# Performance work log

Hardware: AMD Instinct MI355X
Metric: run time of the kernel (lower is better)

Reference implementation:

```python
import jax, jax.numpy as jnp
import numpy as np

N_CLUSTERS = 10

def _conv(x, w, b, stride):
    y = jax.lax.conv_general_dilated(x, w, stride, 'VALID', dimension_numbers=('NCHW', 'OIHW', 'NCHW'))
    return y + b[None, :, None, None]

def _forward(x, conv1_w, conv1_b, conv2_w, conv2_b, conv3_w, conv3_b,
             anc0_w, anc0_b, anc1_w, anc1_b, anc2_w, anc2_b, anc3_w, anc3_b,
             W1_w, W1_b, U_w, U_b, V_w, V_b, Wa_w, Wa_b,
             cluster_w, cluster_b, cls_w, cls_b):
    # backbone: three stride-2 valid convs
    h1 = _conv(x, conv1_w, conv1_b, (2, 2))
    h2 = _conv(h1, conv2_w, conv2_b, (2, 2))
    h3 = _conv(h2, conv3_w, conv3_b, (2, 2))  # [1,512,63,63]
    ancs = [_conv(h3, anc0_w, anc0_b, (1, 1)),
            _conv(h3, anc1_w, anc1_b, (1, 1)),
            _conv(h3, anc2_w, anc2_b, (1, 1)),
            _conv(h3, anc3_w, anc3_b, (1, 1))]
    ksizes = [(3, 3), (1, 1), (3, 1), (1, 3)]
    Hf, Wf = h3.shape[2], h3.shape[3]
    feats, coords = [], []
    # feat_organizer: flatten each anchor map to [Ha*Wa, 1024] and build normalized box coords
    for a, (kh, kw) in zip(ancs, ksizes):
        C, Ha, Wa = a.shape[1], a.shape[2], a.shape[3]
        feats.append(a[0].reshape(C, Ha * Wa).T)
        ys, xs = jnp.meshgrid(jnp.arange(Ha, dtype=jnp.float32), jnp.arange(Wa, dtype=jnp.float32), indexing='ij')
        cx = (xs.reshape(-1) + kw * 0.5) / Wf
        cy = (ys.reshape(-1) + kh * 0.5) / Hf
        bw = jnp.full((Ha * Wa,), kw / Wf, jnp.float32)
        bh = jnp.full((Ha * Wa,), kh / Hf, jnp.float32)
        coords.append(jnp.stack([cx, cy, bw, bh], axis=1))
    feat = jnp.concatenate(feats, 0)      # [N,1024]
    coords = jnp.concatenate(coords, 0)   # [N,4]
    # gated-attention MLP (AttentionHead)
    hmid = jax.nn.relu(feat @ W1_w.T + W1_b)              # [N,512]
    u = jax.nn.sigmoid(hmid @ U_w.T + U_b)                # [N,256]
    v = jnp.tanh(hmid @ V_w.T + V_b)                      # [N,256]
    att = jax.nn.sigmoid((u * v) @ Wa_w.T + Wa_b)[:, 0]   # [N]
    # cluster_features: rank anchors by attention, split into equal clusters,
    # attention-weighted segment reduce of features and box coords per cluster
    N = att.shape[0]
    rank = jnp.argsort(jnp.argsort(-att))
    cid = (rank * N_CLUSTERS) // N                         # [N] int cluster ids
    sw = jax.ops.segment_sum(att, cid, num_segments=N_CLUSTERS)                       # [nc]
    fc = jax.ops.segment_sum(hmid * att[:, None], cid, num_segments=N_CLUSTERS) / (sw[:, None] + 1e-8)   # [nc,512]
    pc = jax.ops.segment_sum(coords * att[:, None], cid, num_segments=N_CLUSTERS) / (sw[:, None] + 1e-8) # [nc,4]
    # ClusterAttention: conv with kernel (1,512) == per-cluster dot product, softmax over clusters
    scores = fc @ cluster_w + cluster_b                    # [nc]
    att_c = jax.nn.softmax(scores)
    # attention_pooling: attention-weighted sum of cluster features
    final = (att_c[:, None] * fc).sum(0, keepdims=True)    # [1,512]
    logits = final @ cls_w.T + cls_b
    return jax.nn.softmax(logits, axis=1), att_c.reshape(1, N_CLUSTERS, 1), pc

def setup_inputs() -> dict:
    key = jax.random.key(0)
    ks = jax.random.split(key, 30)
    def rn(k, shape, scale=0.02):
        return jax.random.normal(k, shape, jnp.float32) * scale
    d = {}
    d['x'] = jax.random.normal(ks[0], (1, 3, 512, 512), jnp.float32)
    d['conv1_w'] = rn(ks[1], (128, 3, 3, 3));    d['conv1_b'] = jnp.zeros((128,), jnp.float32)
    d['conv2_w'] = rn(ks[2], (256, 128, 3, 3));  d['conv2_b'] = jnp.zeros((256,), jnp.float32)
    d['conv3_w'] = rn(ks[3], (512, 256, 3, 3));  d['conv3_b'] = jnp.zeros((512,), jnp.float32)
    d['anc0_w'] = rn(ks[4], (1024, 512, 3, 3));  d['anc0_b'] = jnp.zeros((1024,), jnp.float32)
    d['anc1_w'] = rn(ks[5], (1024, 512, 1, 1));  d['anc1_b'] = jnp.zeros((1024,), jnp.float32)
    d['anc2_w'] = rn(ks[6], (1024, 512, 3, 1));  d['anc2_b'] = jnp.zeros((1024,), jnp.float32)
    d['anc3_w'] = rn(ks[7], (1024, 512, 1, 3));  d['anc3_b'] = jnp.zeros((1024,), jnp.float32)
    d['W1_w'] = rn(ks[8], (512, 1024));          d['W1_b'] = jnp.zeros((512,), jnp.float32)
    d['U_w'] = rn(ks[9], (256, 512));            d['U_b'] = jnp.zeros((256,), jnp.float32)
    d['V_w'] = rn(ks[10], (256, 512));           d['V_b'] = jnp.zeros((256,), jnp.float32)
    d['Wa_w'] = rn(ks[11], (1, 256));            d['Wa_b'] = jnp.zeros((1,), jnp.float32)
    d['cluster_w'] = rn(ks[12], (512,));         d['cluster_b'] = jnp.zeros((), jnp.float32)
    d['cls_w'] = rn(ks[13], (10, 512));          d['cls_b'] = jnp.zeros((10,), jnp.float32)
    return d

def reference(x, conv1_w, conv1_b, conv2_w, conv2_b, conv3_w, conv3_b,
              anc0_w, anc0_b, anc1_w, anc1_b, anc2_w, anc2_b, anc3_w, anc3_b,
              W1_w, W1_b, U_w, U_b, V_w, V_b, Wa_w, Wa_b,
              cluster_w, cluster_b, cls_w, cls_b):
    return _forward(x, conv1_w, conv1_b, conv2_w, conv2_b, conv3_w, conv3_b,
                    anc0_w, anc0_b, anc1_w, anc1_b, anc2_w, anc2_b, anc3_w, anc3_b,
                    W1_w, W1_b, U_w, U_b, V_w, V_b, Wa_w, Wa_b,
                    cluster_w, cluster_b, cls_w, cls_b)
```

## Files before the change

### kernel.cpp

```cpp
#include <hip/hip_runtime.h>
#include <math.h>


#define NTOT 15376
typedef unsigned short u16;
typedef unsigned long long u64;
typedef __attribute__((ext_vector_type(8))) short bf16x8;
typedef __attribute__((ext_vector_type(4))) float f32x4;

static __device__ __forceinline__ u16 f2bf(float x) {
    union { float f; unsigned u; } v; v.f = x;
    unsigned r = v.u + 0x7FFF + ((v.u >> 16) & 1);
    return (u16)(r >> 16);
}
static __device__ __forceinline__ float bf2f(u16 h) {
    union { unsigned u; float f; } v; v.u = ((unsigned)h) << 16;
    return v.f;
}

static __device__ __forceinline__ void glds16(const void* g, void* l) {
    __builtin_amdgcn_global_load_lds(
        (const __attribute__((address_space(1))) void*)g,
        (__attribute__((address_space(3))) void*)l,
        16, 0, 0);
}

__global__ __launch_bounds__(256) void conv1k(
    const float* __restrict__ in, const float* __restrict__ wt,
    const float* __restrict__ bs, u16* __restrict__ h1T)
{
    int sp = blockIdx.x * 256 + threadIdx.x;
    if (sp >= 255 * 255) return;
    int oc0 = blockIdx.y * 16;
    int oy = sp / 255, ox = sp - oy * 255;
    const float* ip = in + (long)oy * 2 * 512 + ox * 2;
    float acc[16];
#pragma unroll
    for (int o = 0; o < 16; ++o) acc[o] = bs[oc0 + o];
#pragma unroll
    for (int ic = 0; ic < 3; ++ic)
#pragma unroll
        for (int ky = 0; ky < 3; ++ky)
#pragma unroll
            for (int kx = 0; kx < 3; ++kx) {
                float x = ip[ic * 262144 + ky * 512 + kx];
                const float* wp = wt + oc0 * 27 + ic * 9 + ky * 3 + kx;
#pragma unroll
                for (int o = 0; o < 16; ++o)
                    acc[o] = fmaf(x, wp[o * 27], acc[o]);
            }
    u16* dst = h1T + (long)sp * 128 + oc0;
#pragma unroll
    for (int g = 0; g < 4; ++g) {
        u64 pk = (u64)f2bf(acc[g * 4 + 0])
               | ((u64)f2bf(acc[g * 4 + 1]) << 16)
               | ((u64)f2bf(acc[g * 4 + 2]) << 32)
               | ((u64)f2bf(acc[g * 4 + 3]) << 48);
        *(u64*)(dst + g * 4) = pk;
    }
}

__global__ __launch_bounds__(256) void pack_all(
    const float* __restrict__ s0, const float* __restrict__ s1,
    const float* __restrict__ s2, const float* __restrict__ s3,
    const float* __restrict__ s4, const float* __restrict__ s5,
    const float* __restrict__ s6, const float* __restrict__ s7,
    const float* __restrict__ s8, u16* __restrict__ dst)
{
    long i = (long)blockIdx.x * 256 + threadIdx.x;
    if (i >= 10649600L) return;
    const long c1 = 4718592L, c2 = 5242880L, c3 = 6815744L, c4 = 8388608L,
               c5 = 8912896L, c7 = 9175040L, c8 = 9469952L;
    if (i >= c5 && i < c7) {
        long loc = i - c5;
        int ic = (int)(loc % 512);
        long row = loc / 512;
        const float* src = (row & 1) ? s6 : s5;
        long j = row >> 1;
        dst[i] = f2bf(src[j * 512 + ic]);
        return;
    }
    const float* src; long base; int IC, NT;
    if      (i < c1) { src = s0; base = 0;  IC = 512;  NT = 9; }
    else if (i < c2) { src = s1; base = c1; IC = 512;  NT = 1; }
    else if (i < c3) { src = s2; base = c2; IC = 512;  NT = 3; }
    else if (i < c4) { src = s3; base = c3; IC = 512;  NT = 3; }
    else if (i < c5) { src = s4; base = c4; IC = 1024; NT = 1; }
    else if (i < c8) { src = s7; base = c7; IC = 128;  NT = 9; }
    else             { src = s8; base = c8; IC = 256;  NT = 9; }
    long loc = i - base;
    int ic = (int)(loc % IC);
    long r = loc / IC;
    int t = (int)(r % NT);
    long oc = r / NT;
    dst[i] = f2bf(src[(oc * IC + ic) * NT + t]);
}

__global__ __launch_bounds__(256) void transp_w(
    const u16* __restrict__ Wpk, u16* __restrict__ WpkT)
{
    __shared__ u16 tile[64][65];
    int bid = blockIdx.x;
    int ocb = bid & 15;
    int rt  = bid >> 4;
    int kbase, rowlen; long sbase;
    if      (rt < 72)  { kbase = 0;    sbase = 0L;       rowlen = 4608; }
    else if (rt < 80)  { kbase = 4608; sbase = 4718592L; rowlen = 512;  }
    else if (rt < 104) { kbase = 5120; sbase = 5242880L; rowlen = 1536; }
    else               { kbase = 6656; sbase = 6815744L; rowlen = 1536; }
    int kloc0 = rt * 64 - kbase;
    int t = threadIdx.x, q = t >> 6, ln = t & 63;
#pragma unroll
    for (int i = 0; i < 16; ++i) {
        int ocl = q * 16 + i;
        tile[ocl][ln] = Wpk[sbase + (long)(ocb * 64 + ocl) * rowlen + kloc0 + ln];
    }
    __syncthreads();
#pragma unroll
    for (int i = 0; i < 16; ++i) {
        int kl = q * 16 + i;
        WpkT[(long)(rt * 64 + kl) * 1024 + ocb * 64 + ln] = tile[ln][kl];
    }
}

__global__ __launch_bounds__(256) void hbias_k(
    const float* __restrict__ W1w, const float* __restrict__ W1b,
    const float* __restrict__ b0, const float* __restrict__ b1,
    const float* __restrict__ b2, const float* __restrict__ b3,
    float* __restrict__ hb)
{
    int w = threadIdx.x >> 6, l = threadIdx.x & 63;
    int idx = blockIdx.x * 4 + w;
    int a = idx >> 9, m = idx & 511;
    const float* ab = (a == 0) ? b0 : (a == 1) ? b1 : (a == 2) ? b2 : b3;
    float s = 0.f;
    for (int j = l; j < 1024; j += 64)
        s = fmaf(W1w[(long)m * 1024 + j], ab[j], s);
#pragma unroll
    for (int d = 1; d < 64; d <<= 1) s += __shfl_xor(s, d, 64);
    if (l == 0) hb[idx] = s + W1b[m];
}

template<int CMODE, int EMODE, int TMODE>
__global__ __launch_bounds__(256) void gemm_bt(
    const u16* __restrict__ A, const u16* __restrict__ B,
    const float* __restrict__ bias0, const float* __restrict__ bias1,
    const float* __restrict__ bias2, const float* __restrict__ bias3,
    void* __restrict__ Cout, int M, int N, int RSB, int Ktot,
    int OH, int OW, int obase)
{
    __shared__ u16 As[4096];
    __shared__ u16 Bs[8192];
    const int tid = threadIdx.x, w = tid >> 6, l = tid & 63;
    const int wr = w >> 1, wc = w & 1;
    const int sl = l & 7, sh = l >> 3, sx = sl ^ sh;

    int n0, m0;
    bool TW3 = false;
    const float* bias = bias0;
    if (TMODE == 8) {
        int anc = blockIdx.x >> 8, sub = blockIdx.x & 255;
        n0 = (sub & 31) * 128; m0 = (sub >> 5) * 64;
        Ktot = (anc == 0) ? 72 : (anc == 1) ? 8 : 24;
        TW3 = (anc == 0 || anc == 3);
        A += (anc == 0) ? 0 : (anc == 1) ? 4608 : (anc == 2) ? 5120 : 6656;
        obase = (anc == 0) ? 0 : (anc == 1) ? 3721 : (anc == 2) ? 7690 : 11533;
        OH = (anc == 0 || anc == 2) ? 61 : 63;
        OW = (anc == 0 || anc == 3) ? 61 : 63;
        bias = bias0 + anc * 512;
    } else {
        n0 = blockIdx.x * 128; m0 = blockIdx.y * 64;
    }
    const long RSA = (TMODE == 8) ? 8192 : (long)Ktot * 64;
    const long RSB2 = (long)RSB * 2;
    constexpr int ICL2 = (TMODE == 5) ? 1 : (TMODE == 6) ? 2 : 3;
    constexpr int ICK  = 1 << ICL2;

    int offB[4], ldsOffB[4], ldsOffA[2];
    const char* aBase[2];
    const char* bBase[4];
#pragma unroll
    for (int j = 0; j < 4; ++j) {
        int r = w * 32 + j * 8 + sh;
        int gn = n0 + r;
        if (CMODE == 0)      { gn = min(gn, 3968);  offB[j] = (gn / 63) * 65 + (gn % 63); }
        else if (CMODE == 1) { offB[j] = min(gn, N - 1); }
        else if (CMODE == 2) { gn = min(gn, 16128); offB[j] = (gn / 127) * 510 + (gn % 127) * 2; }
        else                 { gn = min(gn, 3968);  offB[j] = (gn / 63) * 254 + (gn % 63) * 2; }
        ldsOffB[j] = r * 128;
        bBase[j] = (const char*)B + (long)offB[j] * RSB2 + sx * 16;
    }
#pragma unroll
    for (int j = 0; j < 2; ++j) {
        int r = w * 16 + j * 8 + sh;
        ldsOffA[j] = r * 128;
        aBase[j] = (const char*)A + (long)(m0 + r) * RSA * 2 + sx * 16;
    }

    f32x4 acc[2][4];
#pragma unroll
    for (int a = 0; a < 2; ++a)
#pragma unroll
        for (int b = 0; b < 4; ++b) acc[a][b] = (f32x4){0.f, 0.f, 0.f, 0.f};

    const int NTAPS = Ktot >> ICL2;
    for (int t_ = 0; t_ < NTAPS; ++t_) {
        long tOffB;
        if (TMODE == 8) {
            int trow_;
            if (TW3) { int q_ = (t_ * 11) >> 5; trow_ = q_ * 65 + (t_ - q_ * 3); }
            else       trow_ = t_ * 65;
            tOffB = (long)trow_ * RSB2;
        } else if (TMODE == 4) {
            tOffB = (long)t_ * 1024;
        } else if (TMODE == 5) {
            int q_ = (t_ * 11) >> 5;
            tOffB = (long)(q_ * 255 + (t_ - q_ * 3)) * RSB2;
        } else if (TMODE == 6) {
            int q_ = (t_ * 11) >> 5;
            tOffB = (long)(q_ * 127 + (t_ - q_ * 3)) * RSB2;
        } else {
            tOffB = 0;
        }
        long aOff = (long)t_ * (ICK * 128);
#pragma unroll
        for (int kb = 0; kb < ICK; ++kb) {
#pragma unroll
            for (int j = 0; j < 2; ++j)
                glds16(aBase[j] + aOff + kb * 128, (char*)As + ldsOffA[j]);
#pragma unroll
            for (int j = 0; j < 4; ++j)
                glds16(bBase[j] + tOffB + kb * 128, (char*)Bs + ldsOffB[j]);
            __syncthreads();
#pragma unroll
            for (int kk = 0; kk < 2; ++kk) {
                bf16x8 af[2], bfr[4];
#pragma unroll
                for (int f = 0; f < 2; ++f) {
                    int rm = wr * 32 + f * 16 + (l & 15);
                    af[f] = *(const bf16x8*)((const char*)As + rm * 128 +
                               (((kk * 4 + (l >> 4)) ^ (rm & 7)) * 16));
                }
#pragma unroll
                for (int f = 0; f < 4; ++f) {
                    int rn = wc * 64 + f * 16 + (l & 15);
                    bfr[f] = *(const bf16x8*)((const char*)Bs + rn * 128 +
                               (((kk * 4 + (l >> 4)) ^ (rn & 7)) * 16));
                }
#pragma unroll
                for (int fm = 0; fm < 2; ++fm)
#pragma unroll
                    for (int fn = 0; fn < 4; ++fn)
                        acc[fm][fn] = __builtin_amdgcn_mfma_f32_16x16x32_bf16(
                            af[fm], bfr[fn], acc[fm][fn], 0, 0, 0);
            }
            __syncthreads();
        }
    }

#pragma unroll
    for (int fm = 0; fm < 2; ++fm) {
        int gmb = m0 + wr * 32 + fm * 16 + (l >> 4) * 4;
#pragma unroll
        for (int fn = 0; fn < 4; ++fn) {
            int gn = n0 + wc * 64 + fn * 16 + (l & 15);
            f32x4 v = acc[fm][fn];
            if (EMODE == 2) {
                if (gn < N) {
                    int j0 = gmb >> 1;
                    float u0 = 1.f / (1.f + expf(-(v.x + bias0[j0])));
                    float t0 = tanhf(v.y + bias1[j0]);
                    float u1 = 1.f / (1.f + expf(-(v.z + bias0[j0 + 1])));
                    float t1 = tanhf(v.w + bias1[j0 + 1]);
                    float2 o = { u0 * t0 * bias2[j0], u1 * t1 * bias2[j0 + 1] };
                    *(float2*)((float*)Cout + (long)gn * 256 + j0) = o;
                }
            } else if (EMODE == 3) {
                if (gn < 3969) {
                    int trg = (gn / 63) * 65 + (gn % 63);
                    float4 bv = *(const float4*)(bias + gmb);
                    u64 pk = (u64)f2bf(v.x + bv.x)
                           | ((u64)f2bf(v.y + bv.y) << 16)
                           | ((u64)f2bf(v.z + bv.z) << 32)
                           | ((u64)f2bf(v.w + bv.w) << 48);
                    *(u64*)((u16*)Cout + (long)trg * M + gmb) = pk;
                }
            } else if (EMODE == 4) {
                if (gn < N) {
                    float4 bv = *(const float4*)(bias + gmb);
                    u64 pk = (u64)f2bf(v.x + bv.x)
                           | ((u64)f2bf(v.y + bv.y) << 16)
                           | ((u64)f2bf(v.z + bv.z) << 32)
                           | ((u64)f2bf(v.w + bv.w) << 48);
                    *(u64*)((u16*)Cout + (long)gn * M + gmb) = pk;
                }
            } else if (EMODE == 5) {
                if (gn < 3969) {
                    int oy = gn / 63, ox = gn - oy * 63;
                    if (oy < OH && ox < OW) {
                        int trg = obase + oy * OW + ox;
                        float4 bv = *(const float4*)(bias + gmb);
                        u64 pk = (u64)f2bf(fmaxf(v.x + bv.x, 0.f))
                               | ((u64)f2bf(fmaxf(v.y + bv.y, 0.f)) << 16)
                               | ((u64)f2bf(fmaxf(v.z + bv.z, 0.f)) << 32)
                               | ((u64)f2bf(fmaxf(v.w + bv.w, 0.f)) << 48);
                        *(u64*)((u16*)Cout + (long)trg * M + gmb) = pk;
                    }
                }
            } else {
                if (gn < N) {
                    u64 pk = (u64)f2bf(v.x)
                           | ((u64)f2bf(v.y) << 16)
                           | ((u64)f2bf(v.z) << 32)
                           | ((u64)f2bf(v.w) << 48);
                    *(u64*)((u16*)Cout + (long)gn * M + gmb) = pk;
                }
            }
        }
    }
}

__global__ __launch_bounds__(256) void att_v3(
    const float* __restrict__ UVw, const float* __restrict__ Wab,
    float* __restrict__ att, int* __restrict__ rank, int N)
{
    int t = threadIdx.x, l = t & 63, r = t >> 6;
    int n = blockIdx.x * 4 + r;
    if (t < 4 && blockIdx.x * 4 + t < N) rank[blockIdx.x * 4 + t] = 0;
    if (n >= N) return;
    float4 p = *(const float4*)(UVw + (long)n * 256 + l * 4);
    float s = (p.x + p.y) + (p.z + p.w);
#pragma unroll
    for (int d = 1; d < 64; d <<= 1) s += __shfl_xor(s, d, 64);
    if (l == 0) att[n] = 1.f / (1.f + expf(-(s + Wab[0])));
}

__global__ __launch_bounds__(256) void rank_partial(
    const float* __restrict__ att, int* __restrict__ rank, int N)
{
    __shared__ float sa[1024];
    int n = blockIdx.x * 256 + threadIdx.x;
    int base = blockIdx.y * 1024;
    int cnt = min(1024, N - base);
    for (int t = threadIdx.x; t < cnt; t += 256) sa[t] = att[base + t];
    __syncthreads();
    if (n >= N) return;
    float a = att[n];
    int r = 0;
    for (int t = 0; t < cnt; ++t) {
        float aj = sa[t];
        int j = base + t;
        r += (int)(aj > a) | ((int)(aj == a) & (int)(j < n));
    }
    atomicAdd(&rank[n], r);
}

#define FC_NB 256
#define FC_ROWS 61
__global__ __launch_bounds__(256) void fc_part(
    const u16* __restrict__ Hfeat, const float* __restrict__ att,
    const int* __restrict__ rank, float* __restrict__ fcp, int N)
{
    int t = threadIdx.x, b = blockIdx.x;
    int l = t & 63, r = t >> 6;
    float acc[10][8];
#pragma unroll
    for (int k = 0; k < 10; ++k)
#pragma unroll
        for (int e = 0; e < 8; ++e) acc[k][e] = 0.f;
    int n0 = b * FC_ROWS;
    for (int it = 0; it < 16; ++it) {
        int nl = it * 4 + r;
        int n = n0 + nl;
        if (nl >= FC_ROWS || n >= N) break;
        float a = att[n];
        int c = (rank[n] * 10) / N;
        bf16x8 h8 = *(const bf16x8*)(Hfeat + (long)n * 512 + l * 8);
        float hf[8];
#pragma unroll
        for (int e = 0; e < 8; ++e) hf[e] = bf2f((u16)h8[e]);
#pragma unroll
        for (int k = 0; k < 10; ++k) {
            float sel = (c == k) ? a : 0.f;
#pragma unroll
            for (int e = 0; e < 8; ++e)
                acc[k][e] = fmaf(sel, hf[e], acc[k][e]);
        }
    }
    float* dst = fcp + (long)b * 5120 + l * 8;
#pragma unroll
    for (int k = 0; k < 10; ++k)
#pragma unroll
        for (int e = 0; e < 8; ++e) dst[k * 512 + e] = acc[k][e];
}

__global__ __launch_bounds__(256) void fc_sum(
    const float* __restrict__ fcp, float* __restrict__ fc_raw)
{
    int i = blockIdx.x * 256 + threadIdx.x;
    if (i >= 5120) return;
    float s = 0.f;
    for (int b = 0; b < FC_NB; ++b) s += fcp[(long)b * 5120 + i];
    fc_raw[i] = s;
}

__device__ __forceinline__ void anchor_coords(int n, float& cx, float& cy,
                                              float& bw, float& bh)
{
    int kh, kw, Wa, loc;
    if (n < 3721)       { kh = 3; kw = 3; Wa = 61; loc = n; }
    else if (n < 7690)  { kh = 1; kw = 1; Wa = 63; loc = n - 3721; }
    else if (n < 11533) { kh = 3; kw = 1; Wa = 63; loc = n - 7690; }
    else                { kh = 1; kw = 3; Wa = 61; loc = n - 11533; }
    int iy = loc / Wa, ix = loc - iy * Wa;
    cx = (ix + kw * 0.5f) * (1.f / 63.f);
    cy = (iy + kh * 0.5f) * (1.f / 63.f);
    bw = kw * (1.f / 63.f);
    bh = kh * (1.f / 63.f);
}

__global__ __launch_bounds__(256) void swpc_part(
    const float* __restrict__ att, const int* __restrict__ rank,
    float* __restrict__ prt, int N)
{
    __shared__ float red[4][50];
    int t = threadIdx.x, b = blockIdx.x;
    int n = b * 256 + t;
    int l = t & 63, w = t >> 6;
    float a = 0.f, cx = 0.f, cy = 0.f, bw = 0.f, bh = 0.f;
    int c = -1;
    if (n < N) {
        a = att[n]; c = (rank[n] * 10) / N;
        anchor_coords(n, cx, cy, bw, bh);
    }
#pragma unroll
    for (int k = 0; k < 10; ++k) {
        float sel = (c == k) ? a : 0.f;
        float v[5] = {sel, sel * cx, sel * cy, sel * bw, sel * bh};
#pragma unroll
        for (int d = 0; d < 5; ++d) {
            float x = v[d];
#pragma unroll
            for (int s = 1; s < 64; s <<= 1) x += __shfl_xor(x, s, 64);
            if (l == 0) red[w][k * 5 + d] = x;
        }
    }
    __syncthreads();
    if (t < 50) prt[b * 50 + t] = red[0][t] + red[1][t] + red[2][t] + red[3][t];
}

__global__ __launch_bounds__(512) void final_kernel(
    const float* __restrict__ fc_raw, const float* __restrict__ prt,
    const float* __restrict__ cluster_w, const float* __restrict__ cluster_b,
    const float* __restrict__ cls_w, const float* __restrict__ cls_b,
    float* __restrict__ out)
{
    __shared__ float red[512];
    __shared__ float swpc[50];
    int t = threadIdx.x;
    if (t < 50) {
        float s = 0.f;
        for (int b = 0; b < 61; ++b) s += prt[b * 50 + t];
        swpc[t] = s;
    }
    __syncthreads();
    float fcn[10];
#pragma unroll
    for (int k = 0; k < 10; ++k)
        fcn[k] = fc_raw[k * 512 + t] / (swpc[k * 5] + 1e-8f);
    float cw = cluster_w[t];
    float sc[10];
#pragma unroll
    for (int k = 0; k < 10; ++k) {
        red[t] = fcn[k] * cw;
        __syncthreads();
        for (int s = 256; s > 0; s >>= 1) {
            if (t < s) red[t] += red[t + s];
            __syncthreads();
        }
        sc[k] = red[0] + cluster_b[0];
        __syncthreads();
    }
    float mx = sc[0];
#pragma unroll
    for (int k = 1; k < 10; ++k) mx = fmaxf(mx, sc[k]);
    float se = 0.f;
#pragma unroll
    for (int k = 0; k < 10; ++k) { sc[k] = expf(sc[k] - mx); se += sc[k]; }
    float inv = 1.f / se;
#pragma unroll
    for (int k = 0; k < 10; ++k) sc[k] *= inv;
    float fm = 0.f;
#pragma unroll
    for (int k = 0; k < 10; ++k) fm = fmaf(sc[k], fcn[k], fm);
    float lg[10];
#pragma unroll
    for (int c = 0; c < 10; ++c) {
        red[t] = fm * cls_w[c * 512 + t];
        __syncthreads();
        for (int s = 256; s > 0; s >>= 1) {
            if (t < s) red[t] += red[t + s];
            __syncthreads();
        }
        lg[c] = red[0] + cls_b[c];
        __syncthreads();
    }
    float mx2 = lg[0];
#pragma unroll
    for (int c = 1; c < 10; ++c) mx2 = fmaxf(mx2, lg[c]);
    float se2 = 0.f;
#pragma unroll
    for (int c = 0; c < 10; ++c) { lg[c] = expf(lg[c] - mx2); se2 += lg[c]; }
    float inv2 = 1.f / se2;
    if (t < 10) out[t] = lg[t] * inv2;
    if (t >= 10 && t < 20) out[t] = sc[t - 10];
    if (t >= 20 && t < 60) {
        int i = t - 20;
        int k = i >> 2, d = i & 3;
        out[t] = swpc[k * 5 + 1 + d] / (swpc[k * 5] + 1e-8f);
    }
}

extern "C" void kernel_launch(void* const* d_in, const int* in_sizes, int n_in,
                              void* d_out, int out_size, void* d_ws, size_t ws_size,
                              hipStream_t stream)
{
    const float* x    = (const float*)d_in[0];
    const float* c1w  = (const float*)d_in[1];   const float* c1b = (const float*)d_in[2];
    const float* c2w  = (const float*)d_in[3];   const float* c2b = (const float*)d_in[4];
    const float* c3w  = (const float*)d_in[5];   const float* c3b = (const float*)d_in[6];
    const float* a0w  = (const float*)d_in[7];   const float* a0b = (const float*)d_in[8];
    const float* a1w  = (const float*)d_in[9];   const float* a1b = (const float*)d_in[10];
    const float* a2w  = (const float*)d_in[11];  const float* a2b = (const float*)d_in[12];
    const float* a3w  = (const float*)d_in[13];  const float* a3b = (const float*)d_in[14];
    const float* W1w  = (const float*)d_in[15];  const float* W1b = (const float*)d_in[16];
    const float* Uw   = (const float*)d_in[17];  const float* Ub  = (const float*)d_in[18];
    const float* Vw   = (const float*)d_in[19];  const float* Vb  = (const float*)d_in[20];
    const float* Waw  = (const float*)d_in[21];  const float* Wab = (const float*)d_in[22];
    const float* clw  = (const float*)d_in[23];  const float* clb = (const float*)d_in[24];
    const float* clsw = (const float*)d_in[25];  const float* clsb= (const float*)d_in[26];
    float* out = (float*)d_out;

    float* ws = (float*)d_ws;
    u16*   Hfeat= (u16*)ws;
    u16*   h1T  = (u16*)(ws + 3936256);
    u16*   h2T  = (u16*)(ws + 8097856);
    u16*   h3T  = (u16*)(ws + 10162368);
    float* UVw  = ws + 11243968;
    u16*   Wpk  = (u16*)(ws + 15180224);
    u16*   WpkT = (u16*)(ws + 20505024);
    u16*   WcAll= (u16*)(ws + 24699328);
    float* hb   = ws + 26796480;
    float* att  = ws + 26798528;
    int*   rank = (int*)(ws + 26813904);
    float* fcr  = ws + 26829280;
    float* fcp  = ws + 26834400;
    float* prt  = ws + 28145120;

    u16* W1pk  = Wpk + 8388608;
    u16* UVpk  = Wpk + 8912896;
    u16* Wc2pk = Wpk + 9175040;
    u16* Wc3pk = Wpk + 9469952;

    dim3 blk(256);
    const float* nul = nullptr;

    pack_all<<<dim3(41600), blk, 0, stream>>>(a0w, a1w, a2w, a3w, W1w, Uw, Vw,
                                              c2w, c3w, Wpk);
    transp_w<<<dim3(2048), blk, 0, stream>>>(Wpk, WpkT);
    gemm_bt<1,6,4><<<dim3(4, 128), blk, 0, stream>>>(WpkT, W1pk, nul, nul, nul, nul, WcAll, 8192, 512, 1024, 16, 0, 0, 0);
    hbias_k<<<dim3(512), blk, 0, stream>>>(W1w, W1b, a0b, a1b, a2b, a3b, hb);

    conv1k<<<dim3(255, 8), blk, 0, stream>>>(x, c1w, c1b, h1T);
    gemm_bt<2,4,5><<<dim3(127, 4), blk, 0, stream>>>(Wc2pk, h1T, c2b, nul, nul, nul, h2T, 256, 16129, 128, 18, 0, 0, 0);
    gemm_bt<3,3,6><<<dim3(32, 8),  blk, 0, stream>>>(Wc3pk, h2T, c3b, nul, nul, nul, h3T, 512, 3969, 256, 36, 0, 0, 0);

    gemm_bt<0,5,8><<<dim3(1024), blk, 0, stream>>>(WcAll, h3T, hb, nul, nul, nul, Hfeat, 512, 3969, 512, 0, 0, 0, 0);

    gemm_bt<1,2,1><<<dim3(121, 8), blk, 0, stream>>>(UVpk, Hfeat, Ub, Vb, Waw, nul, UVw, 512, NTOT, 512, 8, 0, 0, 0);

    att_v3<<<dim3(3844), blk, 0, stream>>>(UVw, Wab, att, rank, NTOT);
    rank_partial<<<dim3(61, 16), blk, 0, stream>>>(att, rank, NTOT);
    fc_part<<<dim3(FC_NB), blk, 0, stream>>>(Hfeat, att, rank, fcp, NTOT);
    fc_sum<<<dim3(20), blk, 0, stream>>>(fcp, fcr);
    swpc_part<<<dim3(61), blk, 0, stream>>>(att, rank, prt, NTOT);
    final_kernel<<<dim3(1), dim3(512), 0, stream>>>(fcr, prt, clw, clb, clsw, clsb, out);
}
```

Measured before the change: 327.0 us.

## Split-K the conv3 and 3x3 anchor GEMMs into two halves with combine kernels

Conv3 and the 3x3 anchor GEMM now split their 9-tap reduction into a 4-tap and a 5-tap half. Each half writes fp32 partials to a scratch buffer, and new combine kernels add the halves, apply bias (and relu for the anchor) and pack to bf16. The aim is to double the block count of the low-occupancy conv3 launch and balance the anchor launch, where anchor 0 took nine taps while the others took one to three. The cost is extra fp32 partial traffic and two more launches, and the scratch buffer reuses the h1T region.

```diff
diff --git a/kernel.cpp b/kernel.cpp
--- a/kernel.cpp
+++ b/kernel.cpp
@@ -3,6 +3,7 @@
 
 
 #define NTOT 15376
+#define PHALF 2032128
 typedef unsigned short u16;
 typedef unsigned long long u64;
 typedef __attribute__((ext_vector_type(8))) short bf16x8;
@@ -141,13 +142,45 @@
     if (l == 0) hb[idx] = s + W1b[m];
 }
 
+__global__ __launch_bounds__(256) void combA(
+    const float* __restrict__ P, const float* __restrict__ hb,
+    u16* __restrict__ Hfeat)
+{
+    int row = blockIdx.x;
+    int oy = row / 61, ox = row - oy * 61;
+    long n = (long)(oy * 63 + ox) * 512;
+    int c = threadIdx.x * 2;
+    float2 p0 = *(const float2*)(P + n + c);
+    float2 p1 = *(const float2*)(P + PHALF + n + c);
+    float2 b  = *(const float2*)(hb + c);
+    unsigned pk = (unsigned)f2bf(fmaxf(p0.x + p1.x + b.x, 0.f))
+                | ((unsigned)f2bf(fmaxf(p0.y + p1.y + b.y, 0.f)) << 16);
+    *(unsigned*)(Hfeat + (long)row * 512 + c) = pk;
+}
+
+__global__ __launch_bounds__(256) void comb3(
+    const float* __restrict__ P, const float* __restrict__ bias,
+    u16* __restrict__ h3T)
+{
+    int row = blockIdx.x;
+    int trg = (row / 63) * 65 + row % 63;
+    long n = (long)row * 512;
+    int c = threadIdx.x * 2;
+    float2 q0 = *(const float2*)(P + n + c);
+    float2 q1 = *(const float2*)(P + PHALF + n + c);
+    float2 b  = *(const float2*)(bias + c);
+    unsigned pk = (unsigned)f2bf(q0.x + q1.x + b.x)
+                | ((unsigned)f2bf(q0.y + q1.y + b.y) << 16);
+    *(unsigned*)(h3T + (long)trg * 512 + c) = pk;
+}
+
 template<int CMODE, int EMODE, int TMODE>
 __global__ __launch_bounds__(256) void gemm_bt(
     const u16* __restrict__ A, const u16* __restrict__ B,
     const float* __restrict__ bias0, const float* __restrict__ bias1,
     const float* __restrict__ bias2, const float* __restrict__ bias3,
-    void* __restrict__ Cout, int M, int N, int RSB, int Ktot,
-    int OH, int OW, int obase)
+    void* __restrict__ Cout, float* __restrict__ Pbuf,
+    int M, int N, int RSB, int Ktot, int OH, int OW, int obase)
 {
     __shared__ u16 As[4096];
     __shared__ u16 Bs[8192];
@@ -157,24 +190,39 @@
 
     int n0, m0;
     bool TW3 = false;
+    int part = -1;
+    int tbase = 0;
     const float* bias = bias0;
+    constexpr int ICL2 = (TMODE == 5) ? 1 : (TMODE == 6) ? 2 : 3;
+    constexpr int ICK  = 1 << ICL2;
+    int ntaps;
+
     if (TMODE == 8) {
-        int anc = blockIdx.x >> 8, sub = blockIdx.x & 255;
+        int job = blockIdx.x >> 8, sub = blockIdx.x & 255;
         n0 = (sub & 31) * 128; m0 = (sub >> 5) * 64;
-        Ktot = (anc == 0) ? 72 : (anc == 1) ? 8 : 24;
+        int anc;
+        if      (job == 0) { anc = 0; ntaps = 4; tbase = 0; part = 0; }
+        else if (job == 1) { anc = 0; ntaps = 5; tbase = 4; part = 1; }
+        else if (job == 2) { anc = 1; ntaps = 1; }
+        else if (job == 3) { anc = 2; ntaps = 3; }
+        else               { anc = 3; ntaps = 3; }
         TW3 = (anc == 0 || anc == 3);
         A += (anc == 0) ? 0 : (anc == 1) ? 4608 : (anc == 2) ? 5120 : 6656;
         obase = (anc == 0) ? 0 : (anc == 1) ? 3721 : (anc == 2) ? 7690 : 11533;
         OH = (anc == 0 || anc == 2) ? 61 : 63;
         OW = (anc == 0 || anc == 3) ? 61 : 63;
         bias = bias0 + anc * 512;
+    } else if (TMODE == 6 && EMODE == 7) {
+        int half = blockIdx.y >> 3;
+        n0 = blockIdx.x * 128; m0 = (blockIdx.y & 7) * 64;
+        ntaps = half ? 5 : 4; tbase = half * 4;
+        Cout = (void*)((float*)Cout + (long)half * PHALF);
     } else {
         n0 = blockIdx.x * 128; m0 = blockIdx.y * 64;
+        ntaps = Ktot >> ICL2;
     }
     const long RSA = (TMODE == 8) ? 8192 : (long)Ktot * 64;
     const long RSB2 = (long)RSB * 2;
-    constexpr int ICL2 = (TMODE == 5) ? 1 : (TMODE == 6) ? 2 : 3;
-    constexpr int ICK  = 1 << ICL2;
 
     int offB[4], ldsOffB[4], ldsOffA[2];
     const char* aBase[2];
@@ -203,26 +251,26 @@
 #pragma unroll
         for (int b = 0; b < 4; ++b) acc[a][b] = (f32x4){0.f, 0.f, 0.f, 0.f};
 
-    const int NTAPS = Ktot >> ICL2;
-    for (int t_ = 0; t_ < NTAPS; ++t_) {
+    for (int t_ = 0; t_ < ntaps; ++t_) {
+        int te = t_ + tbase;
         long tOffB;
         if (TMODE == 8) {
             int trow_;
-            if (TW3) { int q_ = (t_ * 11) >> 5; trow_ = q_ * 65 + (t_ - q_ * 3); }
-            else       trow_ = t_ * 65;
+            if (TW3) { int q_ = (te * 11) >> 5; trow_ = q_ * 65 + (te - q_ * 3); }
+            else       trow_ = te * 65;
             tOffB = (long)trow_ * RSB2;
         } else if (TMODE == 4) {
-            tOffB = (long)t_ * 1024;
+            tOffB = (long)te * 1024;
         } else if (TMODE == 5) {
-            int q_ = (t_ * 11) >> 5;
-            tOffB = (long)(q_ * 255 + (t_ - q_ * 3)) * RSB2;
+            int q_ = (te * 11) >> 5;
+            tOffB = (long)(q_ * 255 + (te - q_ * 3)) * RSB2;
         } else if (TMODE == 6) {
-            int q_ = (t_ * 11) >> 5;
-            tOffB = (long)(q_ * 127 + (t_ - q_ * 3)) * RSB2;
+            int q_ = (te * 11) >> 5;
+            tOffB = (long)(q_ * 127 + (te - q_ * 3)) * RSB2;
         } else {
             tOffB = 0;
         }
-        long aOff = (long)t_ * (ICK * 128);
+        long aOff = (long)te * (ICK * 128);
 #pragma unroll
         for (int kb = 0; kb < ICK; ++kb) {
 #pragma unroll
@@ -275,16 +323,6 @@
                     float2 o = { u0 * t0 * bias2[j0], u1 * t1 * bias2[j0 + 1] };
                     *(float2*)((float*)Cout + (long)gn * 256 + j0) = o;
                 }
-            } else if (EMODE == 3) {
-                if (gn < 3969) {
-                    int trg = (gn / 63) * 65 + (gn % 63);
-                    float4 bv = *(const float4*)(bias + gmb);
-                    u64 pk = (u64)f2bf(v.x + bv.x)
-                           | ((u64)f2bf(v.y + bv.y) << 16)
-                           | ((u64)f2bf(v.z + bv.z) << 32)
-                           | ((u64)f2bf(v.w + bv.w) << 48);
-                    *(u64*)((u16*)Cout + (long)trg * M + gmb) = pk;
-                }
             } else if (EMODE == 4) {
                 if (gn < N) {
                     float4 bv = *(const float4*)(bias + gmb);
@@ -295,7 +333,12 @@
                     *(u64*)((u16*)Cout + (long)gn * M + gmb) = pk;
                 }
             } else if (EMODE == 5) {
-                if (gn < 3969) {
+                if (TMODE == 8 && part >= 0) {
+                    if (gn < 3969) {
+                        float4 o = { v.x, v.y, v.z, v.w };
+                        *(float4*)(Pbuf + (long)part * PHALF + (long)gn * 512 + gmb) = o;
+                    }
+                } else if (gn < 3969) {
                     int oy = gn / 63, ox = gn - oy * 63;
                     if (oy < OH && ox < OW) {
                         int trg = obase + oy * OW + ox;
@@ -307,13 +350,18 @@
                         *(u64*)((u16*)Cout + (long)trg * M + gmb) = pk;
                     }
                 }
-            } else {
+            } else if (EMODE == 6) {
                 if (gn < N) {
                     u64 pk = (u64)f2bf(v.x)
                            | ((u64)f2bf(v.y) << 16)
                            | ((u64)f2bf(v.z) << 32)
                            | ((u64)f2bf(v.w) << 48);
                     *(u64*)((u16*)Cout + (long)gn * M + gmb) = pk;
+                }
+            } else {
+                if (gn < 3969) {
+                    float4 o = { v.x, v.y, v.z, v.w };
+                    *(float4*)((float*)Cout + (long)gn * 512 + gmb) = o;
                 }
             }
         }
@@ -544,6 +592,7 @@
     float* ws = (float*)d_ws;
     u16*   Hfeat= (u16*)ws;
     u16*   h1T  = (u16*)(ws + 3936256);
+    float* P    = ws + 3936256;
     u16*   h2T  = (u16*)(ws + 8097856);
     u16*   h3T  = (u16*)(ws + 10162368);
     float* UVw  = ws + 11243968;
@@ -564,20 +613,23 @@
 
     dim3 blk(256);
     const float* nul = nullptr;
+    float* fnul = nullptr;
 
     pack_all<<<dim3(41600), blk, 0, stream>>>(a0w, a1w, a2w, a3w, W1w, Uw, Vw,
                                               c2w, c3w, Wpk);
     transp_w<<<dim3(2048), blk, 0, stream>>>(Wpk, WpkT);
-    gemm_bt<1,6,4><<<dim3(4, 128), blk, 0, stream>>>(WpkT, W1pk, nul, nul, nul, nul, WcAll, 8192, 512, 1024, 16, 0, 0, 0);
+    gemm_bt<1,6,4><<<dim3(4, 128), blk, 0, stream>>>(WpkT, W1pk, nul, nul, nul, nul, WcAll, fnul, 8192, 512, 1024, 16, 0, 0, 0);
     hbias_k<<<dim3(512), blk, 0, stream>>>(W1w, W1b, a0b, a1b, a2b, a3b, hb);
 
     conv1k<<<dim3(255, 8), blk, 0, stream>>>(x, c1w, c1b, h1T);
-    gemm_bt<2,4,5><<<dim3(127, 4), blk, 0, stream>>>(Wc2pk, h1T, c2b, nul, nul, nul, h2T, 256, 16129, 128, 18, 0, 0, 0);
-    gemm_bt<3,3,6><<<dim3(32, 8),  blk, 0, stream>>>(Wc3pk, h2T, c3b, nul, nul, nul, h3T, 512, 3969, 256, 36, 0, 0, 0);
-
-    gemm_bt<0,5,8><<<dim3(1024), blk, 0, stream>>>(WcAll, h3T, hb, nul, nul, nul, Hfeat, 512, 3969, 512, 0, 0, 0, 0);
-
-    gemm_bt<1,2,1><<<dim3(121, 8), blk, 0, stream>>>(UVpk, Hfeat, Ub, Vb, Waw, nul, UVw, 512, NTOT, 512, 8, 0, 0, 0);
+    gemm_bt<2,4,5><<<dim3(127, 4), blk, 0, stream>>>(Wc2pk, h1T, c2b, nul, nul, nul, h2T, fnul, 256, 16129, 128, 18, 0, 0, 0);
+    gemm_bt<3,7,6><<<dim3(32, 16), blk, 0, stream>>>(Wc3pk, h2T, nul, nul, nul, nul, P, fnul, 512, 3969, 256, 36, 0, 0, 0);
+    comb3<<<dim3(3969), blk, 0, stream>>>(P, c3b, h3T);
+
+    gemm_bt<0,5,8><<<dim3(1280), blk, 0, stream>>>(WcAll, h3T, hb, nul, nul, nul, Hfeat, P, 512, 3969, 512, 0, 0, 0, 0);
+    combA<<<dim3(3721), blk, 0, stream>>>(P, hb, Hfeat);
+
+    gemm_bt<1,2,1><<<dim3(121, 8), blk, 0, stream>>>(UVpk, Hfeat, Ub, Vb, Waw, nul, UVw, fnul, 512, NTOT, 512, 8, 0, 0, 0);
 
     att_v3<<<dim3(3844), blk, 0, stream>>>(UVw, Wab, att, rank, NTOT);
     rank_partial<<<dim3(61, 16), blk, 0, stream>>>(att, rank, NTOT);
```

Measured after the change: 313.5 us. 1.04x faster.
